# Optimization experiments

Hardware: AMD Instinct MI355X
Metric: run time of the kernel (lower is better)

Reference implementation:

```python
import jax, jax.numpy as jnp
import numpy as np


def _lstm_layer(x, h0, c0, Wih, Whh, b):
    """PyTorch-convention single-layer LSTM. x:[B,T,I], h0/c0:[B,H].
    Wih:[4H,I], Whh:[4H,H], b:[4H] (b_ih+b_hh folded). Gate order: i,f,g,o."""
    H = h0.shape[-1]
    xp = jnp.einsum('bti,gi->btg', x, Wih) + b          # [B,T,4H] precomputed input proj
    xp_t = jnp.swapaxes(xp, 0, 1)                        # [T,B,4H]

    def step(carry, xt):
        h, c = carry
        g = xt + h @ Whh.T                               # [B,4H]
        i = jax.nn.sigmoid(g[:, 0*H:1*H])
        f = jax.nn.sigmoid(g[:, 1*H:2*H])
        gg = jnp.tanh(g[:, 2*H:3*H])
        o = jax.nn.sigmoid(g[:, 3*H:4*H])
        c = f * c + i * gg
        h = o * jnp.tanh(c)
        return (h, c), h

    (_, _), hs = jax.lax.scan(step, (h0, c0), xp_t)      # hs: [T,B,H]
    return jnp.swapaxes(hs, 0, 1)                        # [B,T,H]


def setup_inputs() -> dict:
    key = jax.random.key(0)
    ks = jax.random.split(key, 16)
    B, T, IN, OUT = 256, 1024, 100, 1
    H0, H1, H2 = 32, 64, 128

    def u(k, shape, fan):
        s = 1.0 / np.sqrt(fan)
        return jax.random.uniform(k, shape, jnp.float32, -s, s)

    inp = {
        'input': jax.random.normal(ks[0], (B, T, IN), jnp.float32),
        'h_0': jnp.zeros((1, B, H0), jnp.float32),
        'c_0': jnp.zeros((1, B, H0), jnp.float32),
        'Wih0': u(ks[1], (4*H0, IN), H0), 'Whh0': u(ks[2], (4*H0, H0), H0), 'b0': u(ks[3], (4*H0,), H0),
        'Wih1': u(ks[4], (4*H1, H0), H1), 'Whh1': u(ks[5], (4*H1, H1), H1), 'b1': u(ks[6], (4*H1,), H1),
        'Wih2': u(ks[7], (4*H2, H1), H2), 'Whh2': u(ks[8], (4*H2, H2), H2), 'b2': u(ks[9], (4*H2,), H2),
        'Wl': u(ks[10], (OUT, H2), H2), 'bl': u(ks[11], (OUT,), H2),
    }
    return inp


def reference(input, h_0, c_0, Wih0, Whh0, b0, Wih1, Whh1, b1, Wih2, Whh2, b2, Wl, bl):
    B = input.shape[0]
    z1 = jnp.zeros((B, 64), input.dtype)
    z2 = jnp.zeros((B, 128), input.dtype)
    r = _lstm_layer(input, h_0[0], c_0[0], Wih0, Whh0, b0)   # [B,T,32]
    r = _lstm_layer(r, z1, z1, Wih1, Whh1, b1)               # [B,T,64]
    r = _lstm_layer(r, z2, z2, Wih2, Whh2, b2)               # [B,T,128]
    out = jnp.tanh(jnp.einsum('bth,oh->bto', r, Wl) + bl)    # [B,T,out_dim]
    return out, r
```

## Files before the change

### kernel.cpp

```cpp
#include <hip/hip_runtime.h>
#include <cmath>

#define TT 1024
#define BB 256
#define GG 16
#define NBLK (BB / GG)

#define LOG2E  1.4426950408889634f
#define LOG2E2 2.8853900817779268f

typedef _Float16 f16x8 __attribute__((ext_vector_type(8)));
typedef float    f32x4 __attribute__((ext_vector_type(4)));
typedef _Float16 half2v __attribute__((ext_vector_type(2)));

__device__ __forceinline__ float fast_rcp(float x) { return __builtin_amdgcn_rcpf(x); }
__device__ __forceinline__ float sig2(float g) { return fast_rcp(1.0f + __builtin_exp2f(-g)); }
__device__ __forceinline__ float th2(float g)  { return 1.0f - 2.0f * fast_rcp(1.0f + __builtin_exp2f(g)); }
__device__ __forceinline__ unsigned pack_f16(float a, float b) {
    half2v h; h.x = (_Float16)a; h.y = (_Float16)b;
    return __builtin_bit_cast(unsigned, h);
}
__device__ __forceinline__ void pin4(uint4& u) {
    asm volatile("" : "+v"(u.x), "+v"(u.y), "+v"(u.z), "+v"(u.w));
}
__device__ __forceinline__ f16x8 h8(uint4 u) { return __builtin_bit_cast(f16x8, u); }
__device__ __forceinline__ void step_barrier() {
    asm volatile("s_waitcnt lgkmcnt(0)" ::: "memory");
    __builtin_amdgcn_s_barrier();
    __builtin_amdgcn_sched_barrier(0);
}

#define MFMA16(a, b, c) __builtin_amdgcn_mfma_f32_16x16x32_f16((a), (b), (c), 0, 0, 0)
#define ZERO4 ((f32x4){0.f, 0.f, 0.f, 0.f})

#define FRAG_PTR(buf, k, col) ((char*)&(buf)[(k) >> 5][(((k) & 31) >> 3) * 16 + (col)] + ((k) & 7) * 2)
#define GFRAG_PTR(base, k, col) ((char*)(base) + ((((k) >> 5) * 64 + (((k) & 31) >> 3) * 16 + (col)) * 16 + ((k) & 7) * 2))

__global__ __launch_bounds__(256) void reorder_wf(
    const float* __restrict__ Wih0, const float* __restrict__ Whh0,
    const float* __restrict__ Wih1, const float* __restrict__ Whh1,
    const float* __restrict__ Wih2, const float* __restrict__ Whh2,
    _Float16* __restrict__ wfA0, _Float16* __restrict__ wfA1,
    _Float16* __restrict__ wfC, int* __restrict__ prog)
{
    int idx = blockIdx.x * 256 + threadIdx.x;
    if (idx < 98304) {
        int j = idx & 7, l = (idx >> 3) & 63, t = idx >> 9;
        int kt = t % 6, g = (t / 6) & 3, w = t / 24;
        int row = g * 128 + 16 * w + (l & 15);
        int k = kt * 32 + ((l >> 4) << 3) + j;
        float sc = (g == 2) ? LOG2E2 : LOG2E;
        float v = (k < 64) ? Wih2[row * 64 + k] : Whh2[row * 128 + (k - 64)];
        wfC[idx] = (_Float16)(v * sc);
    } else if (idx < 118784) {
        int f = idx - 98304;
        int j = f & 7, l = (f >> 3) & 63, t = f >> 9;
        int kt = t % 5, g = (t / 5) & 3, w = t / 20;
        int row = g * 32 + 16 * w + (l & 15);
        int k = kt * 32 + ((l >> 4) << 3) + j;
        float sc = (g == 2) ? LOG2E2 : LOG2E;
        float v = (k < 32)  ? Whh0[row * 32 + k]
                : (k < 132) ? Wih0[row * 100 + (k - 32)] : 0.0f;
        wfA0[f] = (_Float16)(v * sc);
    } else if (idx < 143360) {
        int f = idx - 118784;
        int j = f & 7, l = (f >> 3) & 63, t = f >> 9;
        int kt = t % 3, g = (t / 3) & 3, w = t / 12;
        int row = g * 64 + 16 * w + (l & 15);
        int k = kt * 32 + ((l >> 4) << 3) + j;
        float sc = (g == 2) ? LOG2E2 : LOG2E;
        float v = (k < 32) ? Wih1[row * 32 + k] : Whh1[row * 64 + (k - 32)];
        wfA1[f] = (_Float16)(v * sc);
    } else if (idx < 143376) {
        prog[idx - 143360] = 0;
    }
}

__global__ __launch_bounds__(256) void pack_x(
    const float* __restrict__ x, uint4* __restrict__ xf123,
    uint2* __restrict__ xf4c)
{
    int idx = blockIdx.x * 256 + threadIdx.x;
    if (idx < 16 * 1024 * 3 * 64) {
        int l   = idx & 63;
        int kt  = (idx >> 6) % 3;
        int t   = ((idx >> 6) / 3) & 1023;
        int blk = (idx >> 6) / 3 / 1024;
        int col = l & 15, lq = l >> 4;
        int xidx = kt * 32 + lq * 8;
        const float* xr = x + ((size_t)(blk * GG + col) * TT + t) * 100 + xidx;
        float4 a = *reinterpret_cast<const float4*>(xr);
        float4 b = *reinterpret_cast<const float4*>(xr + 4);
        uint4 u;
        u.x = pack_f16(a.x, a.y); u.y = pack_f16(a.z, a.w);
        u.z = pack_f16(b.x, b.y); u.w = pack_f16(b.z, b.w);
        xf123[idx] = u;
    } else {
        int f = idx - 16 * 1024 * 3 * 64;
        int col = f & 15;
        int t   = (f >> 4) & 1023;
        int blk = f >> 14;
        const float* xr = x + ((size_t)(blk * GG + col) * TT + t) * 100 + 96;
        float4 a = *reinterpret_cast<const float4*>(xr);
        uint2 u; u.x = pack_f16(a.x, a.y); u.y = pack_f16(a.z, a.w);
        xf4c[f] = u;
    }
}

__global__ __attribute__((amdgpu_flat_work_group_size(512, 512),
                          amdgpu_waves_per_eu(1, 2)))
void lstm_mega(const uint4* __restrict__ xf123,
               const uint2* __restrict__ xf4c,
               const _Float16* __restrict__ wfA0,
               const _Float16* __restrict__ wfA1,
               const _Float16* __restrict__ wfC,
               const float* __restrict__ b0_,
               const float* __restrict__ b1_,
               const float* __restrict__ b2_,
               const float* __restrict__ h_0,
               const float* __restrict__ c_0,
               uint4* __restrict__ r1f,
               float* __restrict__ r2,
               int* __restrict__ prog)
{
    const int tid = threadIdx.x;
    const int w = tid >> 6, l = tid & 63;
    const int l15 = l & 15, lq = l >> 4;
    const bool isA = (blockIdx.x < NBLK);
    const int blk = isA ? blockIdx.x : blockIdx.x - NBLK;
    const int b0b = blk * GG;

    __shared__ alignas(16) uint4 H0F[2][1][64];
    __shared__ alignas(16) uint4 H1F[2][2][64];
    __shared__ alignas(16) uint4 H2F[2][4][64];

    if (isA) {
        uint4 afu[20];
        f32x4 biasv[4];
        float c[4] = {0.f, 0.f, 0.f, 0.f};
        int jb = 0;
        if (w < 2) {
            jb = 16 * w + 4 * lq;
            const uint4* wf4 = reinterpret_cast<const uint4*>(wfA0);
            #pragma unroll
            for (int g = 0; g < 4; ++g)
                #pragma unroll
                for (int kt = 0; kt < 5; ++kt) {
                    afu[g * 5 + kt] = wf4[((w * 4 + g) * 5 + kt) * 64 + l];
                    pin4(afu[g * 5 + kt]);
                }
            #pragma unroll
            for (int g = 0; g < 4; ++g) {
                float sc = (g == 2) ? LOG2E2 : LOG2E;
                #pragma unroll
                for (int r = 0; r < 4; ++r)
                    biasv[g][r] = b0_[g * 32 + jb + r] * sc;
            }
            #pragma unroll
            for (int r = 0; r < 4; ++r) c[r] = c_0[(b0b + l15) * 32 + jb + r];
        } else if (w < 6) {
            const int w1 = w - 2;
            jb = 16 * w1 + 4 * lq;
            const uint4* wf4 = reinterpret_cast<const uint4*>(wfA1);
            #pragma unroll
            for (int g = 0; g < 4; ++g)
                #pragma unroll
                for (int kt = 0; kt < 3; ++kt) {
                    afu[g * 3 + kt] = wf4[((w1 * 4 + g) * 3 + kt) * 64 + l];
                    pin4(afu[g * 3 + kt]);
                }
            #pragma unroll
            for (int g = 0; g < 4; ++g) {
                float sc = (g == 2) ? LOG2E2 : LOG2E;
                #pragma unroll
                for (int r = 0; r < 4; ++r)
                    biasv[g][r] = b1_[g * 64 + jb + r] * sc;
            }
        }

        {
            int col = tid >> 5, u = tid & 31;
            *(_Float16*)FRAG_PTR(H0F[0], u, col) =
                (_Float16)h_0[(b0b + col) * 32 + u];
            if (tid < 128) H1F[1][tid >> 6][tid & 63] = (uint4){0, 0, 0, 0};
        }

        uint4 bx0 = {0,0,0,0}, bx1 = {0,0,0,0}, bx2 = {0,0,0,0};
        uint2 bx4 = {0, 0};
        if (w < 2) {
            size_t o = ((size_t)blk * TT) * 3 * 64 + l;
            bx0 = xf123[o]; bx1 = xf123[o + 64]; bx2 = xf123[o + 128];
            bx4 = xf4c[((size_t)blk * TT) * 16 + l15];
        }
        step_barrier();

        for (int m = 0; m <= TT; ++m) {
            const int cur = m & 1, nxt = cur ^ 1;

            if ((m & 3) == 0 && m >= 4 && tid == 0)
                __hip_atomic_store(&prog[blk], m - 1, __ATOMIC_RELEASE,
                                   __HIP_MEMORY_SCOPE_AGENT);

            if (w < 2) {
                uint4 cx0 = bx0, cx1 = bx1, cx2 = bx2;
                uint2 cx4 = bx4;
                if (m + 1 < TT) {
                    size_t o = ((size_t)blk * TT + (m + 1)) * 3 * 64 + l;
                    bx0 = xf123[o]; bx1 = xf123[o + 64]; bx2 = xf123[o + 128];
                    bx4 = xf4c[((size_t)blk * TT + (m + 1)) * 16 + l15];
                }
                if (m < TT) {
                    f16x8 bh = reinterpret_cast<const f16x8*>(&H0F[cur][0][0])[l];
                    uint4 t4;
                    t4.x = (lq == 0) ? cx4.x : 0u; t4.y = (lq == 0) ? cx4.y : 0u;
                    t4.z = 0u; t4.w = 0u;
                    f32x4 accA[4], accB[4];
                    #pragma unroll
                    for (int g = 0; g < 4; ++g) {
                        accA[g] = MFMA16(h8(afu[g * 5 + 0]), bh, biasv[g]);
                        accB[g] = MFMA16(h8(afu[g * 5 + 1]), h8(cx0), ZERO4);
                        accA[g] = MFMA16(h8(afu[g * 5 + 2]), h8(cx1), accA[g]);
                        accB[g] = MFMA16(h8(afu[g * 5 + 3]), h8(cx2), accB[g]);
                        accA[g] = MFMA16(h8(afu[g * 5 + 4]), h8(t4), accA[g]);
                    }
                    float h[4];
                    #pragma unroll
                    for (int r = 0; r < 4; ++r) {
                        float ai  = sig2(accA[0][r] + accB[0][r]);
                        float afg = sig2(accA[1][r] + accB[1][r]);
                        float ag  = th2(accA[2][r] + accB[2][r]);
                        float ao  = sig2(accA[3][r] + accB[3][r]);
                        c[r] = fmaf(afg, c[r], ai * ag);
                        h[r] = ao * th2(c[r] * LOG2E2);
                    }
                    uint2 hp = make_uint2(pack_f16(h[0], h[1]), pack_f16(h[2], h[3]));
                    *(uint2*)FRAG_PTR(H0F[nxt], jb, l15) = hp;
                }
            } else if (w < 6) {
                if (m >= 1) {
                    f16x8 bh0 = reinterpret_cast<const f16x8*>(&H0F[cur][0][0])[l];
                    f16x8 bh1 = reinterpret_cast<const f16x8*>(&H1F[cur][0][0])[l];
                    f16x8 bh2 = reinterpret_cast<const f16x8*>(&H1F[cur][1][0])[l];
                    f32x4 accA[4], accB[4];
                    #pragma unroll
                    for (int g = 0; g < 4; ++g) {
                        accA[g] = MFMA16(h8(afu[g * 3 + 0]), bh0, biasv[g]);
                        accB[g] = MFMA16(h8(afu[g * 3 + 1]), bh1, ZERO4);
                        accA[g] = MFMA16(h8(afu[g * 3 + 2]), bh2, accA[g]);
                    }
                    float h[4];
                    #pragma unroll
                    for (int r = 0; r < 4; ++r) {
                        float ai  = sig2(accA[0][r] + accB[0][r]);
                        float afg = sig2(accA[1][r] + accB[1][r]);
                        float ag  = th2(accA[2][r] + accB[2][r]);
                        float ao  = sig2(accA[3][r] + accB[3][r]);
                        c[r] = fmaf(afg, c[r], ai * ag);
                        h[r] = ao * th2(c[r] * LOG2E2);
                    }
                    uint2 hp = make_uint2(pack_f16(h[0], h[1]), pack_f16(h[2], h[3]));
                    *(uint2*)FRAG_PTR(H1F[nxt], jb, l15) = hp;
                    uint4* base = r1f + ((size_t)blk * TT + (m - 1)) * 128;
                    unsigned long long v =
                        (unsigned long long)hp.x | ((unsigned long long)hp.y << 32);
                    __hip_atomic_store(
                        reinterpret_cast<unsigned long long*>(GFRAG_PTR(base, jb, l15)),
                        v, __ATOMIC_RELAXED, __HIP_MEMORY_SCOPE_AGENT);
                    if ((m & 3) == 3)
                        asm volatile("s_waitcnt vmcnt(0)" ::: "memory");
                }
            }
            step_barrier();
        }
        asm volatile("s_waitcnt vmcnt(0)" ::: "memory");
        __builtin_amdgcn_s_barrier();
        if (tid == 0)
            __hip_atomic_store(&prog[blk], 4096, __ATOMIC_RELEASE,
                               __HIP_MEMORY_SCOPE_AGENT);
    } else {
        const int jb = 16 * w + 4 * lq;
        uint4 af[24];
        {
            const uint4* wf4 = reinterpret_cast<const uint4*>(wfC);
            #pragma unroll
            for (int g = 0; g < 4; ++g)
                #pragma unroll
                for (int kt = 0; kt < 6; ++kt) {
                    af[g * 6 + kt] = wf4[((w * 4 + g) * 6 + kt) * 64 + l];
                    pin4(af[g * 6 + kt]);
                }
        }
        f32x4 biasv[4];
        #pragma unroll
        for (int g = 0; g < 4; ++g) {
            float sc = (g == 2) ? LOG2E2 : LOG2E;
            #pragma unroll
            for (int r = 0; r < 4; ++r)
                biasv[g][r] = b2_[g * 128 + jb + r] * sc;
        }
        if (tid < 256) H2F[0][tid >> 6][tid & 63] = (uint4){0, 0, 0, 0};

        if ((tid & 63) == 0) {
            while (__hip_atomic_load(&prog[blk], __ATOMIC_ACQUIRE,
                                     __HIP_MEMORY_SCOPE_AGENT) < 5)
                __builtin_amdgcn_s_sleep(8);
        }
        __builtin_amdgcn_s_barrier();

        uint4 br0, br1;
        {
            size_t o = ((size_t)blk * TT) * 128 + l;
            br0 = r1f[o]; br1 = r1f[o + 64];
        }
        step_barrier();

        float c[4] = {0.f, 0.f, 0.f, 0.f};

        for (int m = 0; m < TT; ++m) {
            const int cur = m & 1, nxt = cur ^ 1;

            if ((m & 3) == 0 && m > 0) {
                if ((tid & 63) == 0) {
                    const int needed = m + 5;
                    while (__hip_atomic_load(&prog[blk], __ATOMIC_ACQUIRE,
                                             __HIP_MEMORY_SCOPE_AGENT) < needed)
                        __builtin_amdgcn_s_sleep(8);
                }
                __builtin_amdgcn_s_barrier();
            }

            uint4 cr0 = br0, cr1 = br1;
            if (m + 1 < TT) {
                size_t o = ((size_t)blk * TT + (m + 1)) * 128 + l;
                br0 = r1f[o]; br1 = r1f[o + 64];
            }

            f16x8 bh[4];
            #pragma unroll
            for (int kt = 0; kt < 4; ++kt)
                bh[kt] = reinterpret_cast<const f16x8*>(&H2F[cur][kt][0])[l];

            f32x4 accA[4], accB[4];
            #pragma unroll
            for (int g = 0; g < 4; ++g) {
                accA[g] = MFMA16(h8(af[g * 6 + 0]), h8(cr0), biasv[g]);
                accB[g] = MFMA16(h8(af[g * 6 + 1]), h8(cr1), ZERO4);
                accA[g] = MFMA16(h8(af[g * 6 + 2]), bh[0], accA[g]);
                accB[g] = MFMA16(h8(af[g * 6 + 3]), bh[1], accB[g]);
                accA[g] = MFMA16(h8(af[g * 6 + 4]), bh[2], accA[g]);
                accB[g] = MFMA16(h8(af[g * 6 + 5]), bh[3], accB[g]);
            }

            float h[4];
            #pragma unroll
            for (int r = 0; r < 4; ++r) {
                float ai  = sig2(accA[0][r] + accB[0][r]);
                float afg = sig2(accA[1][r] + accB[1][r]);
                float ag  = th2(accA[2][r] + accB[2][r]);
                float ao  = sig2(accA[3][r] + accB[3][r]);
                c[r] = fmaf(afg, c[r], ai * ag);
                h[r] = ao * th2(c[r] * LOG2E2);
            }
            uint2 hp = make_uint2(pack_f16(h[0], h[1]), pack_f16(h[2], h[3]));
            *(uint2*)FRAG_PTR(H2F[nxt], jb, l15) = hp;
            float4 hv = make_float4(h[0], h[1], h[2], h[3]);
            *reinterpret_cast<float4*>(
                r2 + ((size_t)(b0b + l15) * TT + m) * 128 + jb) = hv;
            step_barrier();
        }
    }
}

__global__ __launch_bounds__(256) void final_proj(
    const float* __restrict__ r, const float* __restrict__ Wl,
    const float* __restrict__ bl, float* __restrict__ out)
{
    __shared__ float wl[128];
    const int tid = threadIdx.x;
    if (tid < 128) wl[tid] = Wl[tid];
    __syncthreads();

    const int bt = blockIdx.x * 256 + tid;
    const float4* rr = reinterpret_cast<const float4*>(r + (size_t)bt * 128);
    float a0 = 0.f, a1 = 0.f, a2 = 0.f, a3 = 0.f;
    #pragma unroll
    for (int k = 0; k < 32; ++k) {
        float4 v = rr[k];
        a0 = fmaf(v.x, wl[4 * k + 0], a0);
        a1 = fmaf(v.y, wl[4 * k + 1], a1);
        a2 = fmaf(v.z, wl[4 * k + 2], a2);
        a3 = fmaf(v.w, wl[4 * k + 3], a3);
    }
    out[bt] = tanhf(((a0 + a1) + (a2 + a3)) + bl[0]);
}

extern "C" void kernel_launch(void* const* d_in, const int* in_sizes, int n_in,
                              void* d_out, int out_size, void* d_ws, size_t ws_size,
                              hipStream_t stream) {
    const float* input = (const float*)d_in[0];
    const float* h_0   = (const float*)d_in[1];
    const float* c_0   = (const float*)d_in[2];
    const float* Wih0  = (const float*)d_in[3];
    const float* Whh0  = (const float*)d_in[4];
    const float* b0    = (const float*)d_in[5];
    const float* Wih1  = (const float*)d_in[6];
    const float* Whh1  = (const float*)d_in[7];
    const float* b1    = (const float*)d_in[8];
    const float* Wih2  = (const float*)d_in[9];
    const float* Whh2  = (const float*)d_in[10];
    const float* b2    = (const float*)d_in[11];
    const float* Wl    = (const float*)d_in[12];
    const float* bl    = (const float*)d_in[13];

    float* out = (float*)d_out;
    float* r2  = out + (size_t)BB * TT;

    char* ws = (char*)d_ws;
    uint4*    xf123 = (uint4*)ws;
    uint2*    xf4c  = (uint2*)(ws + 50331648);
    uint4*    r1f   = (uint4*)(ws + 52428800);
    _Float16* wfA0  = (_Float16*)(ws + 85983232);
    _Float16* wfA1  = (_Float16*)(ws + 86024192);
    _Float16* wfC   = (_Float16*)(ws + 86073344);
    int*      prog  = (int*)(ws + 86269952);

    hipLaunchKernelGGL(reorder_wf, dim3(561), dim3(256), 0, stream,
                       Wih0, Whh0, Wih1, Whh1, Wih2, Whh2, wfA0, wfA1, wfC, prog);
    hipLaunchKernelGGL(pack_x, dim3(13312), dim3(256), 0, stream,
                       input, xf123, xf4c);
    hipLaunchKernelGGL(lstm_mega, dim3(2 * NBLK), dim3(512), 0, stream,
                       xf123, xf4c, wfA0, wfA1, wfC, b0, b1, b2, h_0, c_0,
                       r1f, r2, prog);
    hipLaunchKernelGGL(final_proj, dim3(BB * TT / 256), dim3(256), 0, stream,
                       r2, Wl, bl, out);
}
```

Before: 1.547 ms.

## Fuse all three LSTM layers into one block with shared-memory wavefront pipeline

Merges the producer (layers 0-1) and consumer (layer 2) blocks into a single 896-thread block per batch group. Layer 1 now passes its hidden state to layer 2 via shared memory with a one-step skew, instead of a global fragment buffer and atomic progress flags. This removes global-memory handoff, release/acquire polling and the progress buffer. The trade-off is half as many blocks, all layers sharing one CU's SIMDs, and each step gated by a single barrier across 14 waves.

Result: slower. 5.652 ms (+265.3%).

```diff
diff --git a/kernel.cpp b/kernel.cpp
--- a/kernel.cpp
+++ b/kernel.cpp
@@ -34,14 +34,13 @@
 #define ZERO4 ((f32x4){0.f, 0.f, 0.f, 0.f})
 
 #define FRAG_PTR(buf, k, col) ((char*)&(buf)[(k) >> 5][(((k) & 31) >> 3) * 16 + (col)] + ((k) & 7) * 2)
-#define GFRAG_PTR(base, k, col) ((char*)(base) + ((((k) >> 5) * 64 + (((k) & 31) >> 3) * 16 + (col)) * 16 + ((k) & 7) * 2))
 
 __global__ __launch_bounds__(256) void reorder_wf(
     const float* __restrict__ Wih0, const float* __restrict__ Whh0,
     const float* __restrict__ Wih1, const float* __restrict__ Whh1,
     const float* __restrict__ Wih2, const float* __restrict__ Whh2,
     _Float16* __restrict__ wfA0, _Float16* __restrict__ wfA1,
-    _Float16* __restrict__ wfC, int* __restrict__ prog)
+    _Float16* __restrict__ wfC)
 {
     int idx = blockIdx.x * 256 + threadIdx.x;
     if (idx < 98304) {
@@ -71,8 +70,6 @@
         float sc = (g == 2) ? LOG2E2 : LOG2E;
         float v = (k < 32) ? Wih1[row * 32 + k] : Whh1[row * 64 + (k - 32)];
         wfA1[f] = (_Float16)(v * sc);
-    } else if (idx < 143376) {
-        prog[idx - 143360] = 0;
     }
 }
 
@@ -107,190 +104,81 @@
     }
 }
 
-__global__ __attribute__((amdgpu_flat_work_group_size(512, 512),
-                          amdgpu_waves_per_eu(1, 2)))
-void lstm_mega(const uint4* __restrict__ xf123,
-               const uint2* __restrict__ xf4c,
-               const _Float16* __restrict__ wfA0,
-               const _Float16* __restrict__ wfA1,
-               const _Float16* __restrict__ wfC,
-               const float* __restrict__ b0_,
-               const float* __restrict__ b1_,
-               const float* __restrict__ b2_,
-               const float* __restrict__ h_0,
-               const float* __restrict__ c_0,
-               uint4* __restrict__ r1f,
-               float* __restrict__ r2,
-               int* __restrict__ prog)
+__global__ __launch_bounds__(896, 1)
+void lstm_fused(const uint4* __restrict__ xf123,
+                const uint2* __restrict__ xf4c,
+                const _Float16* __restrict__ wfA0,
+                const _Float16* __restrict__ wfA1,
+                const _Float16* __restrict__ wfC,
+                const float* __restrict__ b0_,
+                const float* __restrict__ b1_,
+                const float* __restrict__ b2_,
+                const float* __restrict__ h_0,
+                const float* __restrict__ c_0,
+                float* __restrict__ r2)
 {
+    const int blk = blockIdx.x;
+    const int b0b = blk * GG;
     const int tid = threadIdx.x;
     const int w = tid >> 6, l = tid & 63;
     const int l15 = l & 15, lq = l >> 4;
-    const bool isA = (blockIdx.x < NBLK);
-    const int blk = isA ? blockIdx.x : blockIdx.x - NBLK;
-    const int b0b = blk * GG;
 
     __shared__ alignas(16) uint4 H0F[2][1][64];
     __shared__ alignas(16) uint4 H1F[2][2][64];
     __shared__ alignas(16) uint4 H2F[2][4][64];
 
-    if (isA) {
-        uint4 afu[20];
-        f32x4 biasv[4];
-        float c[4] = {0.f, 0.f, 0.f, 0.f};
-        int jb = 0;
-        if (w < 2) {
-            jb = 16 * w + 4 * lq;
-            const uint4* wf4 = reinterpret_cast<const uint4*>(wfA0);
-            #pragma unroll
-            for (int g = 0; g < 4; ++g)
-                #pragma unroll
-                for (int kt = 0; kt < 5; ++kt) {
-                    afu[g * 5 + kt] = wf4[((w * 4 + g) * 5 + kt) * 64 + l];
-                    pin4(afu[g * 5 + kt]);
-                }
-            #pragma unroll
-            for (int g = 0; g < 4; ++g) {
-                float sc = (g == 2) ? LOG2E2 : LOG2E;
-                #pragma unroll
-                for (int r = 0; r < 4; ++r)
-                    biasv[g][r] = b0_[g * 32 + jb + r] * sc;
-            }
-            #pragma unroll
-            for (int r = 0; r < 4; ++r) c[r] = c_0[(b0b + l15) * 32 + jb + r];
-        } else if (w < 6) {
-            const int w1 = w - 2;
-            jb = 16 * w1 + 4 * lq;
-            const uint4* wf4 = reinterpret_cast<const uint4*>(wfA1);
-            #pragma unroll
-            for (int g = 0; g < 4; ++g)
-                #pragma unroll
-                for (int kt = 0; kt < 3; ++kt) {
-                    afu[g * 3 + kt] = wf4[((w1 * 4 + g) * 3 + kt) * 64 + l];
-                    pin4(afu[g * 3 + kt]);
-                }
-            #pragma unroll
-            for (int g = 0; g < 4; ++g) {
-                float sc = (g == 2) ? LOG2E2 : LOG2E;
-                #pragma unroll
-                for (int r = 0; r < 4; ++r)
-                    biasv[g][r] = b1_[g * 64 + jb + r] * sc;
-            }
+    uint4 afu[24];
+    f32x4 biasv[4];
+    float c[4] = {0.f, 0.f, 0.f, 0.f};
+    int jb = 0;
+    if (w < 2) {
+        jb = 16 * w + 4 * lq;
+        const uint4* wf4 = reinterpret_cast<const uint4*>(wfA0);
+        #pragma unroll
+        for (int g = 0; g < 4; ++g)
+            #pragma unroll
+            for (int kt = 0; kt < 5; ++kt) {
+                afu[g * 5 + kt] = wf4[((w * 4 + g) * 5 + kt) * 64 + l];
+                pin4(afu[g * 5 + kt]);
+            }
+        #pragma unroll
+        for (int g = 0; g < 4; ++g) {
+            float sc = (g == 2) ? LOG2E2 : LOG2E;
+            #pragma unroll
+            for (int r = 0; r < 4; ++r)
+                biasv[g][r] = b0_[g * 32 + jb + r] * sc;
         }
-
-        {
-            int col = tid >> 5, u = tid & 31;
-            *(_Float16*)FRAG_PTR(H0F[0], u, col) =
-                (_Float16)h_0[(b0b + col) * 32 + u];
-            if (tid < 128) H1F[1][tid >> 6][tid & 63] = (uint4){0, 0, 0, 0};
+        #pragma unroll
+        for (int r = 0; r < 4; ++r) c[r] = c_0[(b0b + l15) * 32 + jb + r];
+    } else if (w < 6) {
+        const int w1 = w - 2;
+        jb = 16 * w1 + 4 * lq;
+        const uint4* wf4 = reinterpret_cast<const uint4*>(wfA1);
+        #pragma unroll
+        for (int g = 0; g < 4; ++g)
+            #pragma unroll
+            for (int kt = 0; kt < 3; ++kt) {
+                afu[g * 3 + kt] = wf4[((w1 * 4 + g) * 3 + kt) * 64 + l];
+                pin4(afu[g * 3 + kt]);
+            }
+        #pragma unroll
+        for (int g = 0; g < 4; ++g) {
+            float sc = (g == 2) ? LOG2E2 : LOG2E;
+            #pragma unroll
+            for (int r = 0; r < 4; ++r)
+                biasv[g][r] = b1_[g * 64 + jb + r] * sc;
         }
-
-        uint4 bx0 = {0,0,0,0}, bx1 = {0,0,0,0}, bx2 = {0,0,0,0};
-        uint2 bx4 = {0, 0};
-        if (w < 2) {
-            size_t o = ((size_t)blk * TT) * 3 * 64 + l;
-            bx0 = xf123[o]; bx1 = xf123[o + 64]; bx2 = xf123[o + 128];
-            bx4 = xf4c[((size_t)blk * TT) * 16 + l15];
-        }
-        step_barrier();
-
-        for (int m = 0; m <= TT; ++m) {
-            const int cur = m & 1, nxt = cur ^ 1;
-
-            if ((m & 3) == 0 && m >= 4 && tid == 0)
-                __hip_atomic_store(&prog[blk], m - 1, __ATOMIC_RELEASE,
-                                   __HIP_MEMORY_SCOPE_AGENT);
-
-            if (w < 2) {
-                uint4 cx0 = bx0, cx1 = bx1, cx2 = bx2;
-                uint2 cx4 = bx4;
-                if (m + 1 < TT) {
-                    size_t o = ((size_t)blk * TT + (m + 1)) * 3 * 64 + l;
-                    bx0 = xf123[o]; bx1 = xf123[o + 64]; bx2 = xf123[o + 128];
-                    bx4 = xf4c[((size_t)blk * TT + (m + 1)) * 16 + l15];
-                }
-                if (m < TT) {
-                    f16x8 bh = reinterpret_cast<const f16x8*>(&H0F[cur][0][0])[l];
-                    uint4 t4;
-                    t4.x = (lq == 0) ? cx4.x : 0u; t4.y = (lq == 0) ? cx4.y : 0u;
-                    t4.z = 0u; t4.w = 0u;
-                    f32x4 accA[4], accB[4];
-                    #pragma unroll
-                    for (int g = 0; g < 4; ++g) {
-                        accA[g] = MFMA16(h8(afu[g * 5 + 0]), bh, biasv[g]);
-                        accB[g] = MFMA16(h8(afu[g * 5 + 1]), h8(cx0), ZERO4);
-                        accA[g] = MFMA16(h8(afu[g * 5 + 2]), h8(cx1), accA[g]);
-                        accB[g] = MFMA16(h8(afu[g * 5 + 3]), h8(cx2), accB[g]);
-                        accA[g] = MFMA16(h8(afu[g * 5 + 4]), h8(t4), accA[g]);
-                    }
-                    float h[4];
-                    #pragma unroll
-                    for (int r = 0; r < 4; ++r) {
-                        float ai  = sig2(accA[0][r] + accB[0][r]);
-                        float afg = sig2(accA[1][r] + accB[1][r]);
-                        float ag  = th2(accA[2][r] + accB[2][r]);
-                        float ao  = sig2(accA[3][r] + accB[3][r]);
-                        c[r] = fmaf(afg, c[r], ai * ag);
-                        h[r] = ao * th2(c[r] * LOG2E2);
-                    }
-                    uint2 hp = make_uint2(pack_f16(h[0], h[1]), pack_f16(h[2], h[3]));
-                    *(uint2*)FRAG_PTR(H0F[nxt], jb, l15) = hp;
-                }
-            } else if (w < 6) {
-                if (m >= 1) {
-                    f16x8 bh0 = reinterpret_cast<const f16x8*>(&H0F[cur][0][0])[l];
-                    f16x8 bh1 = reinterpret_cast<const f16x8*>(&H1F[cur][0][0])[l];
-                    f16x8 bh2 = reinterpret_cast<const f16x8*>(&H1F[cur][1][0])[l];
-                    f32x4 accA[4], accB[4];
-                    #pragma unroll
-                    for (int g = 0; g < 4; ++g) {
-                        accA[g] = MFMA16(h8(afu[g * 3 + 0]), bh0, biasv[g]);
-                        accB[g] = MFMA16(h8(afu[g * 3 + 1]), bh1, ZERO4);
-                        accA[g] = MFMA16(h8(afu[g * 3 + 2]), bh2, accA[g]);
-                    }
-                    float h[4];
-                    #pragma unroll
-                    for (int r = 0; r < 4; ++r) {
-                        float ai  = sig2(accA[0][r] + accB[0][r]);
-                        float afg = sig2(accA[1][r] + accB[1][r]);
-                        float ag  = th2(accA[2][r] + accB[2][r]);
-                        float ao  = sig2(accA[3][r] + accB[3][r]);
-                        c[r] = fmaf(afg, c[r], ai * ag);
-                        h[r] = ao * th2(c[r] * LOG2E2);
-                    }
-                    uint2 hp = make_uint2(pack_f16(h[0], h[1]), pack_f16(h[2], h[3]));
-                    *(uint2*)FRAG_PTR(H1F[nxt], jb, l15) = hp;
-                    uint4* base = r1f + ((size_t)blk * TT + (m - 1)) * 128;
-                    unsigned long long v =
-                        (unsigned long long)hp.x | ((unsigned long long)hp.y << 32);
-                    __hip_atomic_store(
-                        reinterpret_cast<unsigned long long*>(GFRAG_PTR(base, jb, l15)),
-                        v, __ATOMIC_RELAXED, __HIP_MEMORY_SCOPE_AGENT);
-                    if ((m & 3) == 3)
-                        asm volatile("s_waitcnt vmcnt(0)" ::: "memory");
-                }
-            }
-            step_barrier();
-        }
-        asm volatile("s_waitcnt vmcnt(0)" ::: "memory");
-        __builtin_amdgcn_s_barrier();
-        if (tid == 0)
-            __hip_atomic_store(&prog[blk], 4096, __ATOMIC_RELEASE,
-                               __HIP_MEMORY_SCOPE_AGENT);
     } else {
-        const int jb = 16 * w + 4 * lq;
-        uint4 af[24];
-        {
-            const uint4* wf4 = reinterpret_cast<const uint4*>(wfC);
-            #pragma unroll
-            for (int g = 0; g < 4; ++g)
-                #pragma unroll
-                for (int kt = 0; kt < 6; ++kt) {
-                    af[g * 6 + kt] = wf4[((w * 4 + g) * 6 + kt) * 64 + l];
-                    pin4(af[g * 6 + kt]);
-                }
-        }
-        f32x4 biasv[4];
+        const int w2 = w - 6;
+        jb = 16 * w2 + 4 * lq;
+        const uint4* wf4 = reinterpret_cast<const uint4*>(wfC);
+        #pragma unroll
+        for (int g = 0; g < 4; ++g)
+            #pragma unroll
+            for (int kt = 0; kt < 6; ++kt) {
+                afu[g * 6 + kt] = wf4[((w2 * 4 + g) * 6 + kt) * 64 + l];
+                pin4(afu[g * 6 + kt]);
+            }
         #pragma unroll
         for (int g = 0; g < 4; ++g) {
             float sc = (g == 2) ? LOG2E2 : LOG2E;
@@ -298,76 +186,126 @@
             for (int r = 0; r < 4; ++r)
                 biasv[g][r] = b2_[g * 128 + jb + r] * sc;
         }
-        if (tid < 256) H2F[0][tid >> 6][tid & 63] = (uint4){0, 0, 0, 0};
-
-        if ((tid & 63) == 0) {
-            while (__hip_atomic_load(&prog[blk], __ATOMIC_ACQUIRE,
-                                     __HIP_MEMORY_SCOPE_AGENT) < 5)
-                __builtin_amdgcn_s_sleep(8);
-        }
-        __builtin_amdgcn_s_barrier();
-
-        uint4 br0, br1;
-        {
-            size_t o = ((size_t)blk * TT) * 128 + l;
-            br0 = r1f[o]; br1 = r1f[o + 64];
+    }
+
+    if (tid < 512) {
+        int col = tid >> 5, u = tid & 31;
+        *(_Float16*)FRAG_PTR(H0F[0], u, col) = (_Float16)h_0[(b0b + col) * 32 + u];
+    }
+    if (tid < 128) H1F[1][tid >> 6][tid & 63] = (uint4){0, 0, 0, 0};
+    if (tid >= 128 && tid < 384) {
+        int f = tid - 128;
+        H2F[0][f >> 6][f & 63] = (uint4){0, 0, 0, 0};
+    }
+
+    uint4 bx0 = {0,0,0,0}, bx1 = {0,0,0,0}, bx2 = {0,0,0,0};
+    uint2 bx4 = {0, 0};
+    if (w < 2) {
+        size_t o = ((size_t)blk * TT) * 3 * 64 + l;
+        bx0 = xf123[o]; bx1 = xf123[o + 64]; bx2 = xf123[o + 128];
+        bx4 = xf4c[((size_t)blk * TT) * 16 + l15];
+    }
+    step_barrier();
+
+    for (int m = 0; m <= TT + 1; ++m) {
+        const int cur = m & 1, nxt = cur ^ 1;
+
+        if (w < 2) {
+            uint4 cx0 = bx0, cx1 = bx1, cx2 = bx2;
+            uint2 cx4 = bx4;
+            if (m + 1 < TT) {
+                size_t o = ((size_t)blk * TT + (m + 1)) * 3 * 64 + l;
+                bx0 = xf123[o]; bx1 = xf123[o + 64]; bx2 = xf123[o + 128];
+                bx4 = xf4c[((size_t)blk * TT + (m + 1)) * 16 + l15];
+            }
+            if (m < TT) {
+                f16x8 bh = reinterpret_cast<const f16x8*>(&H0F[cur][0][0])[l];
+                uint4 t4;
+                t4.x = (lq == 0) ? cx4.x : 0u; t4.y = (lq == 0) ? cx4.y : 0u;
+                t4.z = 0u; t4.w = 0u;
+                f32x4 accA[4], accB[4];
+                #pragma unroll
+                for (int g = 0; g < 4; ++g) {
+                    accA[g] = MFMA16(h8(afu[g * 5 + 0]), bh, biasv[g]);
+                    accB[g] = MFMA16(h8(afu[g * 5 + 1]), h8(cx0), ZERO4);
+                    accA[g] = MFMA16(h8(afu[g * 5 + 2]), h8(cx1), accA[g]);
+                    accB[g] = MFMA16(h8(afu[g * 5 + 3]), h8(cx2), accB[g]);
+                    accA[g] = MFMA16(h8(afu[g * 5 + 4]), h8(t4), accA[g]);
+                }
+                float h[4];
+                #pragma unroll
+                for (int r = 0; r < 4; ++r) {
+                    float ai  = sig2(accA[0][r] + accB[0][r]);
+                    float afg = sig2(accA[1][r] + accB[1][r]);
+                    float ag  = th2(accA[2][r] + accB[2][r]);
+                    float ao  = sig2(accA[3][r] + accB[3][r]);
+                    c[r] = fmaf(afg, c[r], ai * ag);
+                    h[r] = ao * th2(c[r] * LOG2E2);
+                }
+                uint2 hp = make_uint2(pack_f16(h[0], h[1]), pack_f16(h[2], h[3]));
+                *(uint2*)FRAG_PTR(H0F[nxt], jb, l15) = hp;
+            }
+        } else if (w < 6) {
+            if (m >= 1 && m <= TT) {
+                f16x8 bh0 = reinterpret_cast<const f16x8*>(&H0F[cur][0][0])[l];
+                f16x8 bh1 = reinterpret_cast<const f16x8*>(&H1F[cur][0][0])[l];
+                f16x8 bh2 = reinterpret_cast<const f16x8*>(&H1F[cur][1][0])[l];
+                f32x4 accA[4], accB[4];
+                #pragma unroll
+                for (int g = 0; g < 4; ++g) {
+                    accA[g] = MFMA16(h8(afu[g * 3 + 0]), bh0, biasv[g]);
+                    accB[g] = MFMA16(h8(afu[g * 3 + 1]), bh1, ZERO4);
+                    accA[g] = MFMA16(h8(afu[g * 3 + 2]), bh2, accA[g]);
+                }
+                float h[4];
+                #pragma unroll
+                for (int r = 0; r < 4; ++r) {
+                    float ai  = sig2(accA[0][r] + accB[0][r]);
+                    float afg = sig2(accA[1][r] + accB[1][r]);
+                    float ag  = th2(accA[2][r] + accB[2][r]);
+                    float ao  = sig2(accA[3][r] + accB[3][r]);
+                    c[r] = fmaf(afg, c[r], ai * ag);
+                    h[r] = ao * th2(c[r] * LOG2E2);
+                }
+                uint2 hp = make_uint2(pack_f16(h[0], h[1]), pack_f16(h[2], h[3]));
+                *(uint2*)FRAG_PTR(H1F[nxt], jb, l15) = hp;
+            }
+        } else {
+            if (m >= 2) {
+                f16x8 bq0 = reinterpret_cast<const f16x8*>(&H1F[cur][0][0])[l];
+                f16x8 bq1 = reinterpret_cast<const f16x8*>(&H1F[cur][1][0])[l];
+                f16x8 bh0 = reinterpret_cast<const f16x8*>(&H2F[cur][0][0])[l];
+                f16x8 bh1 = reinterpret_cast<const f16x8*>(&H2F[cur][1][0])[l];
+                f16x8 bh2 = reinterpret_cast<const f16x8*>(&H2F[cur][2][0])[l];
+                f16x8 bh3 = reinterpret_cast<const f16x8*>(&H2F[cur][3][0])[l];
+                f32x4 accA[4], accB[4];
+                #pragma unroll
+                for (int g = 0; g < 4; ++g) {
+                    accA[g] = MFMA16(h8(afu[g * 6 + 0]), bq0, biasv[g]);
+                    accB[g] = MFMA16(h8(afu[g * 6 + 1]), bq1, ZERO4);
+                    accA[g] = MFMA16(h8(afu[g * 6 + 2]), bh0, accA[g]);
+                    accB[g] = MFMA16(h8(afu[g * 6 + 3]), bh1, accB[g]);
+                    accA[g] = MFMA16(h8(afu[g * 6 + 4]), bh2, accA[g]);
+                    accB[g] = MFMA16(h8(afu[g * 6 + 5]), bh3, accB[g]);
+                }
+                float h[4];
+                #pragma unroll
+                for (int r = 0; r < 4; ++r) {
+                    float ai  = sig2(accA[0][r] + accB[0][r]);
+                    float afg = sig2(accA[1][r] + accB[1][r]);
+                    float ag  = th2(accA[2][r] + accB[2][r]);
+                    float ao  = sig2(accA[3][r] + accB[3][r]);
+                    c[r] = fmaf(afg, c[r], ai * ag);
+                    h[r] = ao * th2(c[r] * LOG2E2);
+                }
+                uint2 hp = make_uint2(pack_f16(h[0], h[1]), pack_f16(h[2], h[3]));
+                *(uint2*)FRAG_PTR(H2F[nxt], jb, l15) = hp;
+                float4 hv = make_float4(h[0], h[1], h[2], h[3]);
+                *reinterpret_cast<float4*>(
+                    r2 + ((size_t)(b0b + l15) * TT + (m - 2)) * 128 + jb) = hv;
+            }
         }
         step_barrier();
-
-        float c[4] = {0.f, 0.f, 0.f, 0.f};
-
-        for (int m = 0; m < TT; ++m) {
-            const int cur = m & 1, nxt = cur ^ 1;
-
-            if ((m & 3) == 0 && m > 0) {
-                if ((tid & 63) == 0) {
-                    const int needed = m + 5;
-                    while (__hip_atomic_load(&prog[blk], __ATOMIC_ACQUIRE,
-                                             __HIP_MEMORY_SCOPE_AGENT) < needed)
-                        __builtin_amdgcn_s_sleep(8);
-                }
-                __builtin_amdgcn_s_barrier();
-            }
-
-            uint4 cr0 = br0, cr1 = br1;
-            if (m + 1 < TT) {
-                size_t o = ((size_t)blk * TT + (m + 1)) * 128 + l;
-                br0 = r1f[o]; br1 = r1f[o + 64];
-            }
-
-            f16x8 bh[4];
-            #pragma unroll
-            for (int kt = 0; kt < 4; ++kt)
-                bh[kt] = reinterpret_cast<const f16x8*>(&H2F[cur][kt][0])[l];
-
-            f32x4 accA[4], accB[4];
-            #pragma unroll
-            for (int g = 0; g < 4; ++g) {
-                accA[g] = MFMA16(h8(af[g * 6 + 0]), h8(cr0), biasv[g]);
-                accB[g] = MFMA16(h8(af[g * 6 + 1]), h8(cr1), ZERO4);
-                accA[g] = MFMA16(h8(af[g * 6 + 2]), bh[0], accA[g]);
-                accB[g] = MFMA16(h8(af[g * 6 + 3]), bh[1], accB[g]);
-                accA[g] = MFMA16(h8(af[g * 6 + 4]), bh[2], accA[g]);
-                accB[g] = MFMA16(h8(af[g * 6 + 5]), bh[3], accB[g]);
-            }
-
-            float h[4];
-            #pragma unroll
-            for (int r = 0; r < 4; ++r) {
-                float ai  = sig2(accA[0][r] + accB[0][r]);
-                float afg = sig2(accA[1][r] + accB[1][r]);
-                float ag  = th2(accA[2][r] + accB[2][r]);
-                float ao  = sig2(accA[3][r] + accB[3][r]);
-                c[r] = fmaf(afg, c[r], ai * ag);
-                h[r] = ao * th2(c[r] * LOG2E2);
-            }
-            uint2 hp = make_uint2(pack_f16(h[0], h[1]), pack_f16(h[2], h[3]));
-            *(uint2*)FRAG_PTR(H2F[nxt], jb, l15) = hp;
-            float4 hv = make_float4(h[0], h[1], h[2], h[3]);
-            *reinterpret_cast<float4*>(
-                r2 + ((size_t)(b0b + l15) * TT + m) * 128 + jb) = hv;
-            step_barrier();
-        }
     }
 }
 
@@ -418,19 +356,16 @@
     char* ws = (char*)d_ws;
     uint4*    xf123 = (uint4*)ws;
     uint2*    xf4c  = (uint2*)(ws + 50331648);
-    uint4*    r1f   = (uint4*)(ws + 52428800);
-    _Float16* wfA0  = (_Float16*)(ws + 85983232);
-    _Float16* wfA1  = (_Float16*)(ws + 86024192);
-    _Float16* wfC   = (_Float16*)(ws + 86073344);
-    int*      prog  = (int*)(ws + 86269952);
-
-    hipLaunchKernelGGL(reorder_wf, dim3(561), dim3(256), 0, stream,
-                       Wih0, Whh0, Wih1, Whh1, Wih2, Whh2, wfA0, wfA1, wfC, prog);
+    _Float16* wfA0  = (_Float16*)(ws + 52428800);
+    _Float16* wfA1  = (_Float16*)(ws + 52469760);
+    _Float16* wfC   = (_Float16*)(ws + 52518912);
+
+    hipLaunchKernelGGL(reorder_wf, dim3(560), dim3(256), 0, stream,
+                       Wih0, Whh0, Wih1, Whh1, Wih2, Whh2, wfA0, wfA1, wfC);
     hipLaunchKernelGGL(pack_x, dim3(13312), dim3(256), 0, stream,
                        input, xf123, xf4c);
-    hipLaunchKernelGGL(lstm_mega, dim3(2 * NBLK), dim3(512), 0, stream,
-                       xf123, xf4c, wfA0, wfA1, wfC, b0, b1, b2, h_0, c_0,
-                       r1f, r2, prog);
+    hipLaunchKernelGGL(lstm_fused, dim3(NBLK), dim3(896), 0, stream,
+                       xf123, xf4c, wfA0, wfA1, wfC, b0, b1, b2, h_0, c_0, r2);
     hipLaunchKernelGGL(final_proj, dim3(BB * TT / 256), dim3(256), 0, stream,
                        r2, Wl, bl, out);
 }
```
